# Optimization experiments

Hardware: AMD Instinct MI355X
Metric: run time of the kernel (lower is better)

## Reference

```python
import jax, jax.numpy as jnp
import numpy as np

ALPHA = 0.2   # LeakyReLU negative slope
EPS = 1e-8
N_NODES = 100000
N_EDGES = 1600000
D_IN = 128
D_OUT = 128


def setup_inputs() -> dict:
    key = jax.random.key(0)
    k1, k2, k3, k4, k5 = jax.random.split(key, 5)
    h = jax.random.normal(k1, (N_NODES, D_IN), dtype=jnp.float32)
    edge_index = jax.random.randint(k2, (2, N_EDGES), 0, N_NODES, dtype=jnp.int32)
    edge_weight = jax.random.uniform(k3, (N_EDGES,), dtype=jnp.float32)
    # xavier-ish scaled params
    W = jax.random.normal(k4, (D_OUT, D_IN), dtype=jnp.float32) * (1.0 / np.sqrt(D_IN))
    a = jax.random.normal(k5, (1, 2 * D_OUT), dtype=jnp.float32) * (1.0 / np.sqrt(2 * D_OUT))
    return {"h": h, "edge_index": edge_index, "edge_weight": edge_weight, "W": W, "a": a}


def reference(h, edge_index, edge_weight, W, a):
    num_nodes = h.shape[0]
    Wh = h @ W.T                                   # [N, D_OUT]
    src, dst = edge_index[0], edge_index[1]
    d_out = Wh.shape[1]
    a_src = a[0, :d_out]                           # a^T [Wh_i || Wh_j] split into two dots
    a_dst = a[0, d_out:]
    Wh_src = Wh[src]                               # [E, D_OUT] edge gather
    e = Wh_src @ a_src + Wh[dst] @ a_dst           # [E]
    e = jnp.where(e >= 0, e, ALPHA * e)            # LeakyReLU
    e = e * edge_weight
    # segment softmax over edges sharing dst; torch init-to-zero amax => max(seg_max, 0)
    seg_max = jax.ops.segment_max(e, dst, num_segments=num_nodes)
    seg_max = jnp.maximum(seg_max, 0.0)
    ex = jnp.exp(e - seg_max[dst])
    seg_sum = jax.ops.segment_sum(ex, dst, num_segments=num_nodes)
    att = ex / (seg_sum[dst] + EPS)                # [E]
    # weighted scatter-add aggregation (dropout is identity in eval/p=0)
    h_prime = jax.ops.segment_sum(att[:, None] * Wh_src, dst, num_segments=num_nodes)
    return h_prime
```

## Files before the change

kernel.cpp:

```cpp
#include <hip/hip_runtime.h>
#include <hip/hip_bf16.h>
#include <math.h>

#define D_FEAT 128
#define ALPHA 0.2f
#define EPS 1e-8f

#define BSHIFT 7
#define BNODES 128
#define NB_MAX 800
#define NB_PAD 1024
#define CAP_B 2432
#define CCHUNK 2048

typedef __bf16 bf16x8 __attribute__((ext_vector_type(8)));
typedef float f32x4 __attribute__((ext_vector_type(4)));

__device__ __forceinline__ void split_bf16(const float* __restrict__ p,
                                           bf16x8& hi, bf16x8& lo)
{
    f32x4 a = *(const f32x4*)p;
    f32x4 b = *(const f32x4*)(p + 4);
#pragma unroll
    for (int j = 0; j < 4; ++j) {
        float x = a[j]; __bf16 xh = (__bf16)x;
        hi[j] = xh; lo[j] = (__bf16)(x - (float)xh);
        float y = b[j]; __bf16 yh = (__bf16)y;
        hi[j + 4] = yh; lo[j + 4] = (__bf16)(y - (float)yh);
    }
}

__global__ __launch_bounds__(256) void presplit_w(
    const float* __restrict__ W, __bf16* __restrict__ Whi, __bf16* __restrict__ Wlo)
{
    const int i = blockIdx.x * 256 + threadIdx.x;
    const float x = W[i];
    const __bf16 xh = (__bf16)x;
    Whi[i] = xh;
    Wlo[i] = (__bf16)(x - (float)xh);
}

__global__ __launch_bounds__(256) void gemm_s_kernel(
    const float* __restrict__ h,
    const __bf16* __restrict__ Whi, const __bf16* __restrict__ Wlo,
    const float* __restrict__ a, __bf16* __restrict__ Whb,
    float* __restrict__ s_src, float* __restrict__ s_dst, int N)
{
    const int wave = threadIdx.x >> 6;
    const int lane = threadIdx.x & 63;
    const int row0 = blockIdx.x * 128 + wave * 32;
    if (row0 >= N) return;

    const int l15 = lane & 15;
    const int quad = lane >> 4;

    bf16x8 ahi[2][4], alo[2][4];
#pragma unroll
    for (int m = 0; m < 2; ++m) {
        int arow = row0 + m * 16 + l15;
        if (arow >= N) arow = N - 1;
#pragma unroll
        for (int kk = 0; kk < 4; ++kk)
            split_bf16(h + (size_t)arow * D_FEAT + kk * 32 + quad * 8,
                       ahi[m][kk], alo[m][kk]);
    }

    f32x4 acc[2][8];
#pragma unroll
    for (int m = 0; m < 2; ++m)
#pragma unroll
        for (int n = 0; n < 8; ++n) acc[m][n] = (f32x4){0.f, 0.f, 0.f, 0.f};

#pragma unroll
    for (int kk = 0; kk < 4; ++kk) {
#pragma unroll
        for (int n = 0; n < 8; ++n) {
            const size_t boff = (size_t)(n * 16 + l15) * D_FEAT + kk * 32 + quad * 8;
            const bf16x8 bhi = *(const bf16x8*)(Whi + boff);
            const bf16x8 blo = *(const bf16x8*)(Wlo + boff);
#pragma unroll
            for (int m = 0; m < 2; ++m) {
                acc[m][n] = __builtin_amdgcn_mfma_f32_16x16x32_bf16(ahi[m][kk], bhi, acc[m][n], 0, 0, 0);
                acc[m][n] = __builtin_amdgcn_mfma_f32_16x16x32_bf16(ahi[m][kk], blo, acc[m][n], 0, 0, 0);
                acc[m][n] = __builtin_amdgcn_mfma_f32_16x16x32_bf16(alo[m][kk], bhi, acc[m][n], 0, 0, 0);
            }
        }
    }

#pragma unroll
    for (int m = 0; m < 2; ++m) {
        const int rbase = row0 + m * 16;
        float psrc[4] = {0.f, 0.f, 0.f, 0.f};
        float pdst[4] = {0.f, 0.f, 0.f, 0.f};
#pragma unroll
        for (int n = 0; n < 8; ++n) {
            const int col = n * 16 + l15;
            const float as = a[col];
            const float ad = a[D_FEAT + col];
#pragma unroll
            for (int r = 0; r < 4; ++r) {
                const int row = rbase + quad * 4 + r;
                const float v = acc[m][n][r];
                if (row < N) Whb[(size_t)row * D_FEAT + col] = (__bf16)v;
                psrc[r] += v * as;
                pdst[r] += v * ad;
            }
        }
#pragma unroll
        for (int off = 1; off < 16; off <<= 1) {
#pragma unroll
            for (int r = 0; r < 4; ++r) {
                psrc[r] += __shfl_xor(psrc[r], off, 64);
                pdst[r] += __shfl_xor(pdst[r], off, 64);
            }
        }
        if (l15 == 0) {
#pragma unroll
            for (int r = 0; r < 4; ++r) {
                const int row = rbase + quad * 4 + r;
                if (row < N) { s_src[row] = psrc[r]; s_dst[row] = pdst[r]; }
            }
        }
    }
}

__global__ __launch_bounds__(256) void bin_sort_local(
    const int* __restrict__ src, const int* __restrict__ dst,
    const float* __restrict__ ew,
    const float* __restrict__ s_src, const float* __restrict__ s_dst,
    int* __restrict__ gcur, uint2* __restrict__ bin, int E, int NB)
{
    __shared__ uint2 srt[CCHUNK];
    __shared__ unsigned short sbkt[CCHUNK];
    __shared__ int lhist[NB_PAD];
    __shared__ int loff[NB_PAD];
    __shared__ int lcur[NB_PAD];
    __shared__ int gbase[NB_PAD];
    __shared__ int sh[256];

    const int t = threadIdx.x;
    const int i0 = blockIdx.x * CCHUNK + t * 8;

    lhist[t] = 0; lhist[t + 256] = 0; lhist[t + 512] = 0; lhist[t + 768] = 0;
    __syncthreads();

    int n = E - i0; n = n < 0 ? 0 : (n > 8 ? 8 : n);
    int ss[8], dd[8];
    float wwv[8], exv[8];
    unsigned meta[8];
    int bb[8];

    if (n == 8) {
        const int4 sa = *(const int4*)(src + i0);
        const int4 sb = *(const int4*)(src + i0 + 4);
        const int4 da = *(const int4*)(dst + i0);
        const int4 db = *(const int4*)(dst + i0 + 4);
        const float4 wa = *(const float4*)(ew + i0);
        const float4 wb = *(const float4*)(ew + i0 + 4);
        ss[0] = sa.x; ss[1] = sa.y; ss[2] = sa.z; ss[3] = sa.w;
        ss[4] = sb.x; ss[5] = sb.y; ss[6] = sb.z; ss[7] = sb.w;
        dd[0] = da.x; dd[1] = da.y; dd[2] = da.z; dd[3] = da.w;
        dd[4] = db.x; dd[5] = db.y; dd[6] = db.z; dd[7] = db.w;
        wwv[0] = wa.x; wwv[1] = wa.y; wwv[2] = wa.z; wwv[3] = wa.w;
        wwv[4] = wb.x; wwv[5] = wb.y; wwv[6] = wb.z; wwv[7] = wb.w;
    } else {
        for (int k = 0; k < n; ++k) {
            ss[k] = src[i0 + k]; dd[k] = dst[i0 + k]; wwv[k] = ew[i0 + k];
        }
    }
#pragma unroll
    for (int k = 0; k < 8; ++k) {
        if (k < n) {
            const int s = ss[k], d = dd[k];
            float e = s_src[s] + s_dst[d];
            e = (e >= 0.f) ? e : ALPHA * e;
            e *= wwv[k];
            exv[k] = expf(e);
            bb[k] = d >> BSHIFT;
            meta[k] = (unsigned)s | ((unsigned)(d & (BNODES - 1)) << 17);
            atomicAdd(&lhist[bb[k]], 1);
        }
    }
    __syncthreads();

    const int v0 = lhist[4 * t];
    const int v1 = lhist[4 * t + 1];
    const int v2 = lhist[4 * t + 2];
    const int v3 = lhist[4 * t + 3];
    const int ts = v0 + v1 + v2 + v3;
    sh[t] = ts;
    __syncthreads();
    for (int off = 1; off < 256; off <<= 1) {
        int x = (t >= off) ? sh[t - off] : 0;
        __syncthreads();
        sh[t] += x;
        __syncthreads();
    }
    int run = sh[t] - ts;
    loff[4 * t] = run;     lcur[4 * t] = run;     run += v0;
    loff[4 * t + 1] = run; lcur[4 * t + 1] = run; run += v1;
    loff[4 * t + 2] = run; lcur[4 * t + 2] = run; run += v2;
    loff[4 * t + 3] = run; lcur[4 * t + 3] = run;
    const int total = sh[255];

    for (int b = t; b < NB; b += 256) {
        const int c = lhist[b];
        gbase[b] = c ? atomicAdd(&gcur[b], c) : 0;
    }
    __syncthreads();

#pragma unroll
    for (int k = 0; k < 8; ++k) {
        if (k < n) {
            const int p = atomicAdd(&lcur[bb[k]], 1);
            srt[p] = make_uint2(meta[k], __float_as_uint(exv[k]));
            sbkt[p] = (unsigned short)bb[k];
        }
    }
    __syncthreads();

    for (int i = t; i < total; i += 256) {
        const int b = sbkt[i];
        const int gpos = gbase[b] + (i - loff[b]);
        if (gpos < CAP_B)
            bin[(size_t)b * CAP_B + gpos] = srt[i];
    }
}

__global__ __launch_bounds__(512) void sort_aggregate(
    const int* __restrict__ gcur, const uint2* __restrict__ bin,
    const __bf16* __restrict__ Whb, float* __restrict__ out, int N)
{
    __shared__ uint2 srec[CAP_B];
    __shared__ float ssums[BNODES];
    __shared__ int lhist[BNODES];
    __shared__ int loff[BNODES];
    __shared__ int lcur[BNODES];
    __shared__ int sh[BNODES];

    const int t = threadIdx.x;
    const int b = blockIdx.x;
    const size_t base = (size_t)b * CAP_B;
    const int node0 = b << BSHIFT;
    const int nnodes = min(BNODES, N - node0);
    int cnt = gcur[b];
    if (cnt > CAP_B) cnt = CAP_B;

    if (t < BNODES) { lhist[t] = 0; ssums[t] = 0.f; }
    __syncthreads();

    for (int i = t; i < cnt; i += 512)
        atomicAdd(&lhist[(bin[base + i].x >> 17) & (BNODES - 1)], 1);
    __syncthreads();

    int hv = 0;
    if (t < BNODES) { hv = lhist[t]; sh[t] = hv; }
    __syncthreads();
    for (int off = 1; off < BNODES; off <<= 1) {
        int x = (t >= off && t < BNODES) ? sh[t - off] : 0;
        __syncthreads();
        if (t < BNODES) sh[t] += x;
        __syncthreads();
    }
    if (t < BNODES) { loff[t] = sh[t] - hv; lcur[t] = sh[t] - hv; }
    __syncthreads();

    for (int i = t; i < cnt; i += 512) {
        const uint2 r = bin[base + i];
        const unsigned dl = (r.x >> 17) & (BNODES - 1);
        const int p = atomicAdd(&lcur[dl], 1);
        srec[p] = make_uint2(r.x & 0x1FFFFu, r.y);
        atomicAdd(&ssums[dl], __uint_as_float(r.y));
    }
    __syncthreads();

    const int wave = t >> 6;
    const int lane = t & 63;
    const int quad = lane >> 4;
    const int c0 = (lane & 15) * 8;

    for (int nd = wave; nd < nnodes; nd += 8) {
        const int rb = loff[nd];
        const int cnt_n = lhist[nd];
        const float inv = 1.f / (ssums[nd] + EPS);

        float acc[8];
#pragma unroll
        for (int i = 0; i < 8; ++i) acc[i] = 0.f;

        int j = 0;
        for (; j + 15 < cnt_n; j += 16) {
            uint2 m[4];
#pragma unroll
            for (int g = 0; g < 4; ++g) m[g] = srec[rb + j + g * 4 + quad];
            bf16x8 v[4];
#pragma unroll
            for (int g = 0; g < 4; ++g)
                v[g] = *(const bf16x8*)(Whb + (size_t)m[g].x * D_FEAT + c0);
#pragma unroll
            for (int g = 0; g < 4; ++g) {
                const float a0 = __uint_as_float(m[g].y);
#pragma unroll
                for (int i = 0; i < 8; ++i) acc[i] += a0 * (float)v[g][i];
            }
        }
        for (; j + 7 < cnt_n; j += 8) {
            const uint2 m0 = srec[rb + j + quad];
            const uint2 m1 = srec[rb + j + 4 + quad];
            const float a0 = __uint_as_float(m0.y);
            const float a1 = __uint_as_float(m1.y);
            const bf16x8 v0 = *(const bf16x8*)(Whb + (size_t)m0.x * D_FEAT + c0);
            const bf16x8 v1 = *(const bf16x8*)(Whb + (size_t)m1.x * D_FEAT + c0);
#pragma unroll
            for (int i = 0; i < 8; ++i)
                acc[i] += a0 * (float)v0[i] + a1 * (float)v1[i];
        }
        for (; j < cnt_n; j += 4) {
            const int je = j + quad;
            const int jc = je < cnt_n ? je : cnt_n - 1;
            const uint2 m = srec[rb + jc];
            const float a0 = (je < cnt_n) ? __uint_as_float(m.y) : 0.f;
            const bf16x8 v = *(const bf16x8*)(Whb + (size_t)m.x * D_FEAT + c0);
#pragma unroll
            for (int i = 0; i < 8; ++i) acc[i] += a0 * (float)v[i];
        }
#pragma unroll
        for (int i = 0; i < 8; ++i) {
            acc[i] += __shfl_xor(acc[i], 16, 64);
            acc[i] += __shfl_xor(acc[i], 32, 64);
            acc[i] *= inv;
        }
        if (lane < 16) {
            f32x4 r0, r1;
            r0[0] = acc[0]; r0[1] = acc[1]; r0[2] = acc[2]; r0[3] = acc[3];
            r1[0] = acc[4]; r1[1] = acc[5]; r1[2] = acc[6]; r1[3] = acc[7];
            float* po = out + (size_t)(node0 + nd) * D_FEAT + c0;
            *(f32x4*)po = r0;
            *(f32x4*)(po + 4) = r1;
        }
    }
}

extern "C" void kernel_launch(void* const* d_in, const int* in_sizes, int n_in,
                              void* d_out, int out_size, void* d_ws, size_t ws_size,
                              hipStream_t stream) {
    const float* h  = (const float*)d_in[0];
    const int* eidx = (const int*)d_in[1];
    const float* ew = (const float*)d_in[2];
    const float* W  = (const float*)d_in[3];
    const float* a  = (const float*)d_in[4];
    float* out      = (float*)d_out;

    const int N = in_sizes[0] / D_FEAT;
    const int E = in_sizes[2];
    const int* src = eidx;
    const int* dst = eidx + E;

    const int NB = (N + BNODES - 1) / BNODES;

    char* ws = (char*)d_ws;
    size_t off = 0;
    int*    gcur      = (int*)(ws + off);   off += (size_t)NB_MAX * 4;
    float*  s_src     = (float*)(ws + off); off += (size_t)N * 4;
    float*  s_dst     = (float*)(ws + off); off += (size_t)N * 4;
    off = (off + 15) & ~(size_t)15;
    __bf16* Whi       = (__bf16*)(ws + off); off += (size_t)D_FEAT * D_FEAT * 2;
    __bf16* Wlo       = (__bf16*)(ws + off); off += (size_t)D_FEAT * D_FEAT * 2;
    uint2*  bin       = (uint2*)(ws + off);  off += (size_t)NB_MAX * CAP_B * 8;
    __bf16* Whb       = (__bf16*)(ws + off); off += (size_t)N * D_FEAT * 2;

    hipMemsetAsync(gcur, 0, (size_t)NB * 4, stream);

    presplit_w<<<64, 256, 0, stream>>>(W, Whi, Wlo);
    gemm_s_kernel<<<(N + 127) / 128, 256, 0, stream>>>(h, Whi, Wlo, a, Whb, s_src, s_dst, N);
    bin_sort_local<<<(E + CCHUNK - 1) / CCHUNK, 256, 0, stream>>>(
        src, dst, ew, s_src, s_dst, gcur, bin, E, NB);
    sort_aggregate<<<NB, 512, 0, stream>>>(gcur, bin, Whb, out, N);
}
```

Before: 270.5 us.

## Compute attention logits inside aggregation from gathered fp16 rows, drop score precompute

Removes the per-node s_src/s_dst projections from the GEMM and the per-edge score gathers and exp from the bin sort. The aggregation kernel now computes each edge's source dot product from the row it already gathers, plus a per-node destination dot product, then applies exp and accumulates the softmax sum itself. Wh is stored as fp16 instead of bf16. This saves random gathers and an extra pass, at the cost of per-edge shuffle reductions in the hot loop. It also exponentiates without subtracting the segment max, which risks overflow on inputs with large logits.

Result: slower. 290.3 us (+7.4%).

```diff
diff --git a/kernel.cpp b/kernel.cpp
--- a/kernel.cpp
+++ b/kernel.cpp
@@ -14,6 +14,8 @@
 #define CCHUNK 2048
 
 typedef __bf16 bf16x8 __attribute__((ext_vector_type(8)));
+typedef _Float16 f16x8 __attribute__((ext_vector_type(8)));
+typedef _Float16 f16x2 __attribute__((ext_vector_type(2)));
 typedef float f32x4 __attribute__((ext_vector_type(4)));
 
 __device__ __forceinline__ void split_bf16(const float* __restrict__ p,
@@ -43,8 +45,7 @@
 __global__ __launch_bounds__(256) void gemm_s_kernel(
     const float* __restrict__ h,
     const __bf16* __restrict__ Whi, const __bf16* __restrict__ Wlo,
-    const float* __restrict__ a, __bf16* __restrict__ Whb,
-    float* __restrict__ s_src, float* __restrict__ s_dst, int N)
+    _Float16* __restrict__ Whf, int N)
 {
     const int wave = threadIdx.x >> 6;
     const int lane = threadIdx.x & 63;
@@ -90,35 +91,13 @@
 #pragma unroll
     for (int m = 0; m < 2; ++m) {
         const int rbase = row0 + m * 16;
-        float psrc[4] = {0.f, 0.f, 0.f, 0.f};
-        float pdst[4] = {0.f, 0.f, 0.f, 0.f};
 #pragma unroll
         for (int n = 0; n < 8; ++n) {
             const int col = n * 16 + l15;
-            const float as = a[col];
-            const float ad = a[D_FEAT + col];
 #pragma unroll
             for (int r = 0; r < 4; ++r) {
                 const int row = rbase + quad * 4 + r;
-                const float v = acc[m][n][r];
-                if (row < N) Whb[(size_t)row * D_FEAT + col] = (__bf16)v;
-                psrc[r] += v * as;
-                pdst[r] += v * ad;
-            }
-        }
-#pragma unroll
-        for (int off = 1; off < 16; off <<= 1) {
-#pragma unroll
-            for (int r = 0; r < 4; ++r) {
-                psrc[r] += __shfl_xor(psrc[r], off, 64);
-                pdst[r] += __shfl_xor(pdst[r], off, 64);
-            }
-        }
-        if (l15 == 0) {
-#pragma unroll
-            for (int r = 0; r < 4; ++r) {
-                const int row = rbase + quad * 4 + r;
-                if (row < N) { s_src[row] = psrc[r]; s_dst[row] = pdst[r]; }
+                if (row < N) Whf[(size_t)row * D_FEAT + col] = (_Float16)acc[m][n][r];
             }
         }
     }
@@ -127,7 +106,6 @@
 __global__ __launch_bounds__(256) void bin_sort_local(
     const int* __restrict__ src, const int* __restrict__ dst,
     const float* __restrict__ ew,
-    const float* __restrict__ s_src, const float* __restrict__ s_dst,
     int* __restrict__ gcur, uint2* __restrict__ bin, int E, int NB)
 {
     __shared__ uint2 srt[CCHUNK];
@@ -146,7 +124,7 @@
 
     int n = E - i0; n = n < 0 ? 0 : (n > 8 ? 8 : n);
     int ss[8], dd[8];
-    float wwv[8], exv[8];
+    float wwv[8];
     unsigned meta[8];
     int bb[8];
 
@@ -171,13 +149,9 @@
 #pragma unroll
     for (int k = 0; k < 8; ++k) {
         if (k < n) {
-            const int s = ss[k], d = dd[k];
-            float e = s_src[s] + s_dst[d];
-            e = (e >= 0.f) ? e : ALPHA * e;
-            e *= wwv[k];
-            exv[k] = expf(e);
+            const int d = dd[k];
             bb[k] = d >> BSHIFT;
-            meta[k] = (unsigned)s | ((unsigned)(d & (BNODES - 1)) << 17);
+            meta[k] = (unsigned)ss[k] | ((unsigned)(d & (BNODES - 1)) << 17);
             atomicAdd(&lhist[bb[k]], 1);
         }
     }
@@ -213,7 +187,7 @@
     for (int k = 0; k < 8; ++k) {
         if (k < n) {
             const int p = atomicAdd(&lcur[bb[k]], 1);
-            srt[p] = make_uint2(meta[k], __float_as_uint(exv[k]));
+            srt[p] = make_uint2(meta[k], __float_as_uint(wwv[k]));
             sbkt[p] = (unsigned short)bb[k];
         }
     }
@@ -229,10 +203,10 @@
 
 __global__ __launch_bounds__(512) void sort_aggregate(
     const int* __restrict__ gcur, const uint2* __restrict__ bin,
-    const __bf16* __restrict__ Whb, float* __restrict__ out, int N)
+    const _Float16* __restrict__ Whf, const float* __restrict__ a,
+    float* __restrict__ out, int N)
 {
     __shared__ uint2 srec[CAP_B];
-    __shared__ float ssums[BNODES];
     __shared__ int lhist[BNODES];
     __shared__ int loff[BNODES];
     __shared__ int lcur[BNODES];
@@ -246,7 +220,7 @@
     int cnt = gcur[b];
     if (cnt > CAP_B) cnt = CAP_B;
 
-    if (t < BNODES) { lhist[t] = 0; ssums[t] = 0.f; }
+    if (t < BNODES) lhist[t] = 0;
     __syncthreads();
 
     for (int i = t; i < cnt; i += 512)
@@ -270,7 +244,6 @@
         const unsigned dl = (r.x >> 17) & (BNODES - 1);
         const int p = atomicAdd(&lcur[dl], 1);
         srec[p] = make_uint2(r.x & 0x1FFFFu, r.y);
-        atomicAdd(&ssums[dl], __uint_as_float(r.y));
     }
     __syncthreads();
 
@@ -279,51 +252,85 @@
     const int quad = lane >> 4;
     const int c0 = (lane & 15) * 8;
 
+    float asv[8];
+#pragma unroll
+    for (int i = 0; i < 8; ++i) asv[i] = a[c0 + i];
+    const float ad0 = a[D_FEAT + 2 * lane];
+    const float ad1 = a[D_FEAT + 2 * lane + 1];
+
     for (int nd = wave; nd < nnodes; nd += 8) {
         const int rb = loff[nd];
         const int cnt_n = lhist[nd];
-        const float inv = 1.f / (ssums[nd] + EPS);
+        const int node = node0 + nd;
+
+        const f16x2 dv = *(const f16x2*)(Whf + (size_t)node * D_FEAT + 2 * lane);
+        float sd = (float)dv[0] * ad0 + (float)dv[1] * ad1;
+#pragma unroll
+        for (int off = 1; off < 64; off <<= 1)
+            sd += __shfl_xor(sd, off, 64);
 
         float acc[8];
 #pragma unroll
         for (int i = 0; i < 8; ++i) acc[i] = 0.f;
+        float ssum = 0.f;
 
         int j = 0;
         for (; j + 15 < cnt_n; j += 16) {
             uint2 m[4];
 #pragma unroll
             for (int g = 0; g < 4; ++g) m[g] = srec[rb + j + g * 4 + quad];
-            bf16x8 v[4];
+            f16x8 v[4];
 #pragma unroll
             for (int g = 0; g < 4; ++g)
-                v[g] = *(const bf16x8*)(Whb + (size_t)m[g].x * D_FEAT + c0);
+                v[g] = *(const f16x8*)(Whf + (size_t)m[g].x * D_FEAT + c0);
 #pragma unroll
             for (int g = 0; g < 4; ++g) {
-                const float a0 = __uint_as_float(m[g].y);
-#pragma unroll
-                for (int i = 0; i < 8; ++i) acc[i] += a0 * (float)v[g][i];
+                float vf[8];
+#pragma unroll
+                for (int i = 0; i < 8; ++i) vf[i] = (float)v[g][i];
+                float dp = vf[0] * asv[0];
+#pragma unroll
+                for (int i = 1; i < 8; ++i) dp += vf[i] * asv[i];
+                dp += __shfl_xor(dp, 1, 64);
+                dp += __shfl_xor(dp, 2, 64);
+                dp += __shfl_xor(dp, 4, 64);
+                dp += __shfl_xor(dp, 8, 64);
+                float e = dp + sd;
+                e = (e >= 0.f) ? e : ALPHA * e;
+                e *= __uint_as_float(m[g].y);
+                const float ex = __expf(e);
+                ssum += ex;
+#pragma unroll
+                for (int i = 0; i < 8; ++i) acc[i] += ex * vf[i];
             }
-        }
-        for (; j + 7 < cnt_n; j += 8) {
-            const uint2 m0 = srec[rb + j + quad];
-            const uint2 m1 = srec[rb + j + 4 + quad];
-            const float a0 = __uint_as_float(m0.y);
-            const float a1 = __uint_as_float(m1.y);
-            const bf16x8 v0 = *(const bf16x8*)(Whb + (size_t)m0.x * D_FEAT + c0);
-            const bf16x8 v1 = *(const bf16x8*)(Whb + (size_t)m1.x * D_FEAT + c0);
-#pragma unroll
-            for (int i = 0; i < 8; ++i)
-                acc[i] += a0 * (float)v0[i] + a1 * (float)v1[i];
         }
         for (; j < cnt_n; j += 4) {
             const int je = j + quad;
             const int jc = je < cnt_n ? je : cnt_n - 1;
             const uint2 m = srec[rb + jc];
-            const float a0 = (je < cnt_n) ? __uint_as_float(m.y) : 0.f;
-            const bf16x8 v = *(const bf16x8*)(Whb + (size_t)m.x * D_FEAT + c0);
-#pragma unroll
-            for (int i = 0; i < 8; ++i) acc[i] += a0 * (float)v[i];
-        }
+            const f16x8 v = *(const f16x8*)(Whf + (size_t)m.x * D_FEAT + c0);
+            float vf[8];
+#pragma unroll
+            for (int i = 0; i < 8; ++i) vf[i] = (float)v[i];
+            float dp = vf[0] * asv[0];
+#pragma unroll
+            for (int i = 1; i < 8; ++i) dp += vf[i] * asv[i];
+            dp += __shfl_xor(dp, 1, 64);
+            dp += __shfl_xor(dp, 2, 64);
+            dp += __shfl_xor(dp, 4, 64);
+            dp += __shfl_xor(dp, 8, 64);
+            float e = dp + sd;
+            e = (e >= 0.f) ? e : ALPHA * e;
+            e *= __uint_as_float(m.y);
+            float ex = __expf(e);
+            if (je >= cnt_n) ex = 0.f;
+            ssum += ex;
+#pragma unroll
+            for (int i = 0; i < 8; ++i) acc[i] += ex * vf[i];
+        }
+        ssum += __shfl_xor(ssum, 16, 64);
+        ssum += __shfl_xor(ssum, 32, 64);
+        const float inv = 1.f / (ssum + EPS);
 #pragma unroll
         for (int i = 0; i < 8; ++i) {
             acc[i] += __shfl_xor(acc[i], 16, 64);
@@ -334,7 +341,7 @@
             f32x4 r0, r1;
             r0[0] = acc[0]; r0[1] = acc[1]; r0[2] = acc[2]; r0[3] = acc[3];
             r1[0] = acc[4]; r1[1] = acc[5]; r1[2] = acc[6]; r1[3] = acc[7];
-            float* po = out + (size_t)(node0 + nd) * D_FEAT + c0;
+            float* po = out + (size_t)node * D_FEAT + c0;
             *(f32x4*)po = r0;
             *(f32x4*)(po + 4) = r1;
         }
@@ -360,20 +367,18 @@
 
     char* ws = (char*)d_ws;
     size_t off = 0;
-    int*    gcur      = (int*)(ws + off);   off += (size_t)NB_MAX * 4;
-    float*  s_src     = (float*)(ws + off); off += (size_t)N * 4;
-    float*  s_dst     = (float*)(ws + off); off += (size_t)N * 4;
+    int*      gcur = (int*)(ws + off);      off += (size_t)NB_MAX * 4;
     off = (off + 15) & ~(size_t)15;
-    __bf16* Whi       = (__bf16*)(ws + off); off += (size_t)D_FEAT * D_FEAT * 2;
-    __bf16* Wlo       = (__bf16*)(ws + off); off += (size_t)D_FEAT * D_FEAT * 2;
-    uint2*  bin       = (uint2*)(ws + off);  off += (size_t)NB_MAX * CAP_B * 8;
-    __bf16* Whb       = (__bf16*)(ws + off); off += (size_t)N * D_FEAT * 2;
+    __bf16*   Whi  = (__bf16*)(ws + off);   off += (size_t)D_FEAT * D_FEAT * 2;
+    __bf16*   Wlo  = (__bf16*)(ws + off);   off += (size_t)D_FEAT * D_FEAT * 2;
+    uint2*    bin  = (uint2*)(ws + off);    off += (size_t)NB_MAX * CAP_B * 8;
+    _Float16* Whf  = (_Float16*)(ws + off); off += (size_t)N * D_FEAT * 2;
 
     hipMemsetAsync(gcur, 0, (size_t)NB * 4, stream);
 
     presplit_w<<<64, 256, 0, stream>>>(W, Whi, Wlo);
-    gemm_s_kernel<<<(N + 127) / 128, 256, 0, stream>>>(h, Whi, Wlo, a, Whb, s_src, s_dst, N);
+    gemm_s_kernel<<<(N + 127) / 128, 256, 0, stream>>>(h, Whi, Wlo, Whf, N);
     bin_sort_local<<<(E + CCHUNK - 1) / CCHUNK, 256, 0, stream>>>(
-        src, dst, ew, s_src, s_dst, gcur, bin, E, NB);
-    sort_aggregate<<<NB, 512, 0, stream>>>(gcur, bin, Whb, out, N);
-}
+        src, dst, ew, gcur, bin, E, NB);
+    sort_aggregate<<<NB, 512, 0, stream>>>(gcur, bin, Whf, a, out, N);
+}
```
